# Optimization experiments

Hardware: AMD Instinct MI355X
Metric: run time of the kernel (lower is better)

The kernel has to match this reference:

```python
import jax, jax.numpy as jnp
import numpy as np

B, T, C, H, NT = 1, 1024, 768, 12, 8
D = C // H  # 64
POWER_ITERS = 4
DP_TEMP = 0.8
ESR_GAMMA = 0.02
ESR_ALPHA = 0.1


def rmsnorm(x, w, eps=1e-6):
    rms = jax.lax.rsqrt(jnp.mean(x * x, axis=-1, keepdims=True) + eps)
    return x * rms * w


def setup_inputs():
    key = jax.random.key(0)
    k0, k1, k2 = jax.random.split(key, 3)
    return {
        "x": jax.random.normal(k0, (B, T, C), jnp.float32),
        "W_qkvg": jax.random.normal(k1, (4 * C, C), jnp.float32) * 0.02,
        "W_out": jax.random.normal(k2, (C, C), jnp.float32) * 0.02,
        "lam": jnp.float32(1.5),
        "log_tau": -0.5 * jnp.ones((H, NT), jnp.float32),
        "logit_w": jnp.zeros((H, NT), jnp.float32),
        "beta": 1.5 * jnp.ones((H,), jnp.float32),
        "out_scale": jnp.ones((H,), jnp.float32),
        "dp_scale": jnp.ones((H,), jnp.float32),
        "logk_scale": jnp.ones((H,), jnp.float32),
        "dt_logit": jnp.float32(np.log(1.0 / 1e-8)),  # dt=1.0 -> logit = log(dt/(1-dt+1e-8))
        "g_norm_w": jnp.ones((D,), jnp.float32),
    }


def reference(x, W_qkvg, W_out, lam, log_tau, logit_w, beta, out_scale,
              dp_scale, logk_scale, dt_logit, g_norm_w):
    # qkvg projection and head split
    qkvg = x @ W_qkvg.T                                    # [B,T,4C]
    q, k, v, g = jnp.split(qkvg, 4, axis=-1)
    to_heads = lambda t: t.reshape(B, T, H, D).transpose(0, 2, 1, 3)  # [B,H,T,D]
    q, k, v, g = map(to_heads, (q, k, v, g))
    g = rmsnorm(g, g_norm_w)

    # pairwise squared distance ||g_i - g_j||^2
    g2 = jnp.sum(g * g, axis=-1)                           # [B,H,T]
    s = jnp.maximum(g2[..., :, None] + g2[..., None, :]
                    - 2.0 * jnp.einsum('bhid,bhjd->bhij', g, g), 0.0)  # [B,H,T,T]

    # fractional log-kernel: logsumexp_t[-(beta/2) log1p(s/(4 tau_t)) + log w_t]
    tau = jnp.maximum(jnp.exp(log_tau), 1e-6)              # [H,NT]
    w = jax.nn.softmax(logit_w, axis=-1)                   # [H,NT]
    beta_c = jnp.clip(beta, 0.5, 2.5)                      # [H]
    log_k_per = -(beta_c[None, :, None, None, None] / 2.0) * jnp.log1p(
        s[:, :, None] / (4.0 * tau[None, :, :, None, None]))          # [B,H,NT,T,T]
    logK = jax.nn.logsumexp(log_k_per + jnp.log(w + 1e-12)[None, :, :, None, None], axis=2)
    logK = logK * logk_scale[None, :, None, None]

    # dot-product scores
    dp = jnp.einsum('bhid,bhjd->bhij', q, k) * (dp_scale[None, :, None, None]
                                                / (np.sqrt(D) * DP_TEMP))

    # causal Markov normalize: blend, mask, stable row-softmax
    mask = jnp.tril(jnp.ones((T, T), bool))[None, None]    # [1,1,T,T]
    blended = lam * dp + (1.0 - lam) * logK
    blended = jnp.where(mask, blended, -jnp.inf)
    mx = jnp.max(blended, axis=-1, keepdims=True)
    mx = jnp.where(jnp.isfinite(mx), mx, 0.0)
    Kmat = jnp.exp(jnp.maximum(blended - mx, -60.0)) * mask
    P = Kmat / jnp.maximum(Kmat.sum(-1, keepdims=True), 1e-12)

    # power iteration for left stationary pi with full-support teleport
    pi0 = jnp.full((B, H, 1, T), 1.0 / T, P.dtype)
    def step(pi, _):
        p = (1.0 - ESR_GAMMA) * (pi @ P) + ESR_GAMMA / T
        p = p / jnp.maximum(p.sum(-1, keepdims=True), 1e-12)
        return p, None
    pi, _ = jax.lax.scan(step, pi0, None, length=POWER_ITERS)
    pi = jax.lax.stop_gradient(pi[..., 0, :])              # [B,H,T] (detached)

    # causal approximation to additive reversibilization
    P_adj = (pi[..., None, :] / jnp.maximum(pi[..., :, None], 1e-12)) \
            * jnp.swapaxes(P, -1, -2)                      # P*_ij = (pi_j/pi_i) P_ji
    P_rev = 0.5 * (P + P_adj) * mask
    P_rev = P_rev / jnp.maximum(P_rev.sum(-1, keepdims=True), 1e-12)

    dt = jax.nn.sigmoid(dt_logit)
    alpha = ESR_ALPHA * dt                                  # scale_alpha_by_dt=True
    P_fin = (1.0 - alpha) * P + alpha * P_rev

    y = (P_fin @ v) * out_scale[None, :, None, None]       # [B,H,T,D]
    y = y.transpose(0, 2, 1, 3).reshape(B, T, C)
    return y @ W_out.T
```

## Files before the change

### kernel.cpp

```cpp
#include <hip/hip_runtime.h>
#include <math.h>

#define TSEQ 1024
#define CD   768
#define HN   12
#define DD   64

#define OFF_QH     0
#define OFF_KH     393216
#define OFF_GH     786432
#define OFF_VHT    1179648
#define OFF_VH     1572864
#define OFF_G2     1966080
#define OFF_YB     1978368
#define OFF_CONSTS 2371584
#define OFF_OPART  2372096
#define OFF_LS     3158528
#define OFF_PD     3170816
#define OFF_XB     3183104
#define OFF_WQB    3576320
#define OFF_WOB    4755968
#define NZERO4     199680

#define N_XB  786432
#define N_WQB 2359296
#define N_WOB 589824

typedef __bf16 bf16x8 __attribute__((ext_vector_type(8)));
typedef float  f32x4  __attribute__((ext_vector_type(4)));
typedef unsigned short u16x8 __attribute__((ext_vector_type(8)));
typedef unsigned short u16x4 __attribute__((ext_vector_type(4)));

__device__ inline unsigned short f2bf(float f) {
  unsigned int u = __float_as_uint(f);
  return (unsigned short)((u + 0x7fffu + ((u >> 16) & 1u)) >> 16);
}
__device__ inline float bf2f(unsigned short u) {
  return __uint_as_float((unsigned)u << 16);
}


__global__ __launch_bounds__(64) void prep_kernel(
    const float* __restrict__ lam_p, const float* __restrict__ log_tau,
    const float* __restrict__ logit_w, const float* __restrict__ beta,
    const float* __restrict__ out_scale, const float* __restrict__ dp_scale,
    const float* __restrict__ logk_scale, const float* __restrict__ dt_logit,
    float* __restrict__ consts) {
  int h = threadIdx.x;
  if (h == 0) {
    float dt = 1.0f / (1.0f + __expf(-dt_logit[0]));
    consts[288] = 0.1f * dt;
  }
  if (h < HN) {
    float lam = lam_p[0];
    float* c = consts + h * 24;
    c[0] = lam * dp_scale[h] * (1.0f / 6.4f);
    c[1] = (1.0f - lam) * logk_scale[h];
    float b = fminf(fmaxf(beta[h], 0.5f), 2.5f);
    c[2] = 0.5f * b;
    c[3] = out_scale[h];
    float m = -1e30f;
    float lw[8];
    bool uni = true;
    for (int t = 0; t < 8; t++) {
      lw[t] = logit_w[h * 8 + t];
      m = fmaxf(m, lw[t]);
      if (log_tau[h * 8 + t] != log_tau[h * 8] || lw[t] != lw[0]) uni = false;
    }
    float s = 0.f;
    float e[8];
    for (int t = 0; t < 8; t++) { e[t] = __expf(lw[t] - m); s += e[t]; }
    for (int t = 0; t < 8; t++) {
      float w = e[t] / s;
      c[12 + t] = log2f(w + 1e-12f);
      float tau = fmaxf(__expf(log_tau[h * 8 + t]), 1e-6f);
      c[4 + t] = 1.0f / (4.0f * tau);
    }
    c[20] = uni ? 1.0f : 8.0f;
  }
}

__global__ __launch_bounds__(256) void zero_kernel(float4* __restrict__ p, int n4) {
  int i = blockIdx.x * 256 + threadIdx.x;
  for (; i < n4; i += gridDim.x * 256) p[i] = make_float4(0.f, 0.f, 0.f, 0.f);
}

__global__ __launch_bounds__(256) void convert_kernel(
    const float* __restrict__ x, const float* __restrict__ wq,
    const float* __restrict__ wo, unsigned short* __restrict__ xb,
    unsigned short* __restrict__ wqb, unsigned short* __restrict__ wob) {
  int i8 = (blockIdx.x * 256 + threadIdx.x) * 8;
  const float* src;
  unsigned short* dst;
  int off;
  if (i8 < N_XB) { src = x; dst = xb; off = i8; }
  else if (i8 < N_XB + N_WQB) { src = wq; dst = wqb; off = i8 - N_XB; }
  else if (i8 < N_XB + N_WQB + N_WOB) { src = wo; dst = wob; off = i8 - N_XB - N_WQB; }
  else return;
  float4 a = *(const float4*)&src[off];
  float4 b = *(const float4*)&src[off + 4];
  u16x8 u;
  u[0] = f2bf(a.x); u[1] = f2bf(a.y); u[2] = f2bf(a.z); u[3] = f2bf(a.w);
  u[4] = f2bf(b.x); u[5] = f2bf(b.y); u[6] = f2bf(b.z); u[7] = f2bf(b.w);
  *(u16x8*)&dst[off] = u;
}

__global__ __launch_bounds__(256, 2) void gemm_qkvg_fused(
    const unsigned short* __restrict__ A, const unsigned short* __restrict__ B,
    const float* __restrict__ consts, const float* __restrict__ g_norm_w,
    unsigned short* __restrict__ qh, unsigned short* __restrict__ kh,
    unsigned short* __restrict__ gh, unsigned short* __restrict__ vh,
    unsigned short* __restrict__ vhT, float* __restrict__ g2) {
  const int K = 768;
  __shared__ __align__(16) unsigned short As[128 * 72];
  __shared__ __align__(16) unsigned short Bs[64 * 72];
  int t = threadIdx.x;
  int lane = t & 63, w = t >> 6;
  int quad = lane >> 4, tx = lane & 15;
  int n0 = blockIdx.x * 64, m0 = blockIdx.y * 128;

  f32x4 acc[2][4] = {};
  int r_ = t >> 3, c8 = (t & 7) * 8;

  for (int k0 = 0; k0 < K; k0 += 64) {
    __syncthreads();
#pragma unroll
    for (int rep = 0; rep < 4; rep++) {
      int r = rep * 32 + r_;
      *(u16x8*)&As[r * 72 + c8] = *(const u16x8*)&A[(size_t)(m0 + r) * K + k0 + c8];
    }
#pragma unroll
    for (int rep = 0; rep < 2; rep++) {
      int r = rep * 32 + r_;
      *(u16x8*)&Bs[r * 72 + c8] = *(const u16x8*)&B[(size_t)(n0 + r) * K + k0 + c8];
    }
    __syncthreads();

#pragma unroll
    for (int ks = 0; ks < 2; ks++) {
      bf16x8 af[2];
#pragma unroll
      for (int mi = 0; mi < 2; mi++)
        af[mi] = *(const bf16x8*)&As[(32 * w + mi * 16 + tx) * 72 + ks * 32 + quad * 8];
#pragma unroll
      for (int ni = 0; ni < 4; ni++) {
        bf16x8 bv = *(const bf16x8*)&Bs[(ni * 16 + tx) * 72 + ks * 32 + quad * 8];
#pragma unroll
        for (int mi = 0; mi < 2; mi++)
          acc[mi][ni] = __builtin_amdgcn_mfma_f32_16x16x32_bf16(af[mi], bv, acc[mi][ni], 0, 0, 0);
      }
    }
  }

  int typ = n0 / CD;
  int h = (n0 - typ * CD) >> 6;
  unsigned short* Ls = As;
  __syncthreads();

  if (typ == 3) {
    float gw4[4];
#pragma unroll
    for (int ni = 0; ni < 4; ni++) gw4[ni] = g_norm_w[ni * 16 + tx];
#pragma unroll
    for (int mi = 0; mi < 2; mi++) {
#pragma unroll
      for (int reg = 0; reg < 4; reg++) {
        float s1 = acc[mi][0][reg] * acc[mi][0][reg] + acc[mi][1][reg] * acc[mi][1][reg]
                 + acc[mi][2][reg] * acc[mi][2][reg] + acc[mi][3][reg] * acc[mi][3][reg];
#pragma unroll
        for (int m = 1; m < 16; m <<= 1) s1 += __shfl_xor(s1, m, 64);
        float rms = rsqrtf(s1 * (1.f / 64.f) + 1e-6f);
        int rl = 32 * w + mi * 16 + quad * 4 + reg;
        float s2 = 0.f;
#pragma unroll
        for (int ni = 0; ni < 4; ni++) {
          float v = acc[mi][ni][reg] * rms * gw4[ni];
          unsigned short us = f2bf(v);
          Ls[rl * 72 + ni * 16 + tx] = us;
          float vb = bf2f(us);
          s2 += vb * vb;
        }
#pragma unroll
        for (int m = 1; m < 16; m <<= 1) s2 += __shfl_xor(s2, m, 64);
        if (tx == 0) g2[h * 1024 + m0 + rl] = s2;
      }
    }
    __syncthreads();
#pragma unroll
    for (int rep = 0; rep < 4; rep++) {
      int idx = rep * 256 + t;
      int r = idx >> 3, cc = (idx & 7) * 8;
      *(u16x8*)&gh[(size_t)(h * 1024 + m0 + r) * 64 + cc] = *(const u16x8*)&Ls[r * 72 + cc];
    }
  } else {
    float sc = (typ == 0) ? consts[h * 24] * 1.44269504089f : 1.0f;
#pragma unroll
    for (int mi = 0; mi < 2; mi++)
#pragma unroll
      for (int ni = 0; ni < 4; ni++)
#pragma unroll
        for (int reg = 0; reg < 4; reg++) {
          int rl = 32 * w + mi * 16 + quad * 4 + reg;
          Ls[rl * 72 + ni * 16 + tx] = f2bf(acc[mi][ni][reg] * sc);
        }
    __syncthreads();
    unsigned short* dst = (typ == 0) ? qh : ((typ == 1) ? kh : vh);
#pragma unroll
    for (int rep = 0; rep < 4; rep++) {
      int idx = rep * 256 + t;
      int r = idx >> 3, cc = (idx & 7) * 8;
      *(u16x8*)&dst[(size_t)(h * 1024 + m0 + r) * 64 + cc] = *(const u16x8*)&Ls[r * 72 + cc];
    }
    if (typ == 2) {
#pragma unroll
      for (int rep = 0; rep < 4; rep++) {
        int idx = rep * 256 + t;
        int d = idx >> 4, rc = (idx & 15) * 8;
        u16x8 u;
#pragma unroll
        for (int j = 0; j < 8; j++) u[j] = Ls[(rc + j) * 72 + d];
        *(u16x8*)&vhT[(size_t)(h * 64 + d) * 1024 + m0 + rc] = u;
      }
    }
  }
}

__global__ __launch_bounds__(256, 2) void gemm_bf16_abT(
    const unsigned short* __restrict__ A, const unsigned short* __restrict__ B,
    float* __restrict__ Cm, int M, int N, int K) {
  __shared__ __align__(16) unsigned short As[128 * 72];
  __shared__ __align__(16) unsigned short Bs[64 * 72];
  int t = threadIdx.x;
  int lane = t & 63, w = t >> 6;
  int quad = lane >> 4, tx = lane & 15;
  int n0 = blockIdx.x * 64, m0 = blockIdx.y * 128;

  f32x4 acc[2][4] = {};
  int r_ = t >> 3, c8 = (t & 7) * 8;

  for (int k0 = 0; k0 < K; k0 += 64) {
    __syncthreads();
#pragma unroll
    for (int rep = 0; rep < 4; rep++) {
      int r = rep * 32 + r_;
      *(u16x8*)&As[r * 72 + c8] = *(const u16x8*)&A[(size_t)(m0 + r) * K + k0 + c8];
    }
#pragma unroll
    for (int rep = 0; rep < 2; rep++) {
      int r = rep * 32 + r_;
      *(u16x8*)&Bs[r * 72 + c8] = *(const u16x8*)&B[(size_t)(n0 + r) * K + k0 + c8];
    }
    __syncthreads();

#pragma unroll
    for (int ks = 0; ks < 2; ks++) {
      bf16x8 af[2];
#pragma unroll
      for (int mi = 0; mi < 2; mi++)
        af[mi] = *(const bf16x8*)&As[(32 * w + mi * 16 + tx) * 72 + ks * 32 + quad * 8];
#pragma unroll
      for (int ni = 0; ni < 4; ni++) {
        bf16x8 bv = *(const bf16x8*)&Bs[(ni * 16 + tx) * 72 + ks * 32 + quad * 8];
#pragma unroll
        for (int mi = 0; mi < 2; mi++)
          acc[mi][ni] = __builtin_amdgcn_mfma_f32_16x16x32_bf16(af[mi], bv, acc[mi][ni], 0, 0, 0);
      }
    }
  }

#pragma unroll
  for (int mi = 0; mi < 2; mi++)
#pragma unroll
    for (int ni = 0; ni < 4; ni++)
#pragma unroll
      for (int reg = 0; reg < 4; reg++) {
        int row = m0 + 32 * w + mi * 16 + quad * 4 + reg;
        Cm[(size_t)row * N + n0 + ni * 16 + tx] = acc[mi][ni][reg];
      }
}

__global__ __launch_bounds__(256, 4) void flash_kernel(
    const unsigned short* __restrict__ qh, const unsigned short* __restrict__ kh,
    const unsigned short* __restrict__ gh, const unsigned short* __restrict__ vhT,
    const float* __restrict__ g2, const float* __restrict__ consts,
    float* __restrict__ Opart, float* __restrict__ lsp, float* __restrict__ pdp) {
  int h = blockIdx.y;
  int uu = 143 - (int)blockIdx.x;
  int it = 0, rem = uu;
  for (it = 0; it < 32; ++it) {
    int njt_ = (it >> 1) + 1;
    int nc = (njt_ + 1) >> 1;
    if (rem < nc) break;
    rem -= nc;
  }
  int njt = (it >> 1) + 1;
  int jt0 = rem * 2;
  int jt1 = (jt0 + 2 < njt) ? (jt0 + 2) : njt;
  bool owns_diag = (jt1 == njt);
  int i0 = it * 32;
  int t = threadIdx.x;
  int lane = t & 63, w = t >> 6;
  int quad = lane >> 4, tx = lane & 15;
  int mi = w >> 1, nb = (w & 1) * 2;

  __shared__ __align__(16) unsigned short Qa[32 * 72];
  __shared__ __align__(16) unsigned short Ga[32 * 72];
  __shared__ __align__(16) unsigned short Ks[64 * 72];
  __shared__ __align__(16) unsigned short GV[64 * 72];
  __shared__ __align__(16) unsigned short psh[32 * 72];
  __shared__ float g2i[32], g2j[64], pdiag[32];

  const float* ch = consts + h * 24;
  float lkc = ch[1], bh2 = ch[2];
  int ntt = (int)ch[20];
  float i4t0 = ch[4];
  float inv4tau[8], logw[8];
#pragma unroll
  for (int tt = 0; tt < 8; tt++) { inv4tau[tt] = ch[4 + tt]; logw[tt] = ch[12 + tt]; }

  {
    int r = t >> 3, c8 = (t & 7) * 8;
    *(u16x8*)&Qa[r * 72 + c8] = *(const u16x8*)&qh[(size_t)(h * 1024 + i0 + r) * 64 + c8];
    *(u16x8*)&Ga[r * 72 + c8] = *(const u16x8*)&gh[(size_t)(h * 1024 + i0 + r) * 64 + c8];
  }
  if (t < 32) { g2i[t] = g2[h * 1024 + i0 + t]; pdiag[t] = 0.f; }
  __syncthreads();

  bf16x8 aq[2], ag[2];
#pragma unroll
  for (int ks = 0; ks < 2; ks++) {
    aq[ks] = *(const bf16x8*)&Qa[(mi * 16 + tx) * 72 + ks * 32 + quad * 8];
    ag[ks] = *(const bf16x8*)&Ga[(mi * 16 + tx) * 72 + ks * 32 + quad * 8];
  }

  f32x4 Oc[2] = {};
  float rowacc[4] = {0.f, 0.f, 0.f, 0.f};
  int r4 = t >> 2, cb = (t & 3) * 16;

  for (int jt = jt0; jt < jt1; jt++) {
    int j0 = jt * 64;
    __syncthreads();
    {
      const unsigned short* kp = &kh[(size_t)(h * 1024 + j0 + r4) * 64 + cb];
      const unsigned short* gp = &gh[(size_t)(h * 1024 + j0 + r4) * 64 + cb];
      *(u16x8*)&Ks[r4 * 72 + cb] = *(const u16x8*)kp;
      *(u16x8*)&Ks[r4 * 72 + cb + 8] = *(const u16x8*)(kp + 8);
      *(u16x8*)&GV[r4 * 72 + cb] = *(const u16x8*)gp;
      *(u16x8*)&GV[r4 * 72 + cb + 8] = *(const u16x8*)(gp + 8);
    }
    if (t < 64) g2j[t] = g2[h * 1024 + j0 + t];
    __syncthreads();

    u16x8 v0, v1;
    {
      const unsigned short* vp = &vhT[(size_t)(h * 64 + r4) * 1024 + j0 + cb];
      v0 = *(const u16x8*)vp;
      v1 = *(const u16x8*)(vp + 8);
    }

    f32x4 sqk[2] = {}, sgg[2] = {};
#pragma unroll
    for (int ni2 = 0; ni2 < 2; ni2++) {
#pragma unroll
      for (int ks = 0; ks < 2; ks++) {
        bf16x8 bk = *(const bf16x8*)&Ks[((nb + ni2) * 16 + tx) * 72 + ks * 32 + quad * 8];
        sqk[ni2] = __builtin_amdgcn_mfma_f32_16x16x32_bf16(aq[ks], bk, sqk[ni2], 0, 0, 0);
        bf16x8 bg = *(const bf16x8*)&GV[((nb + ni2) * 16 + tx) * 72 + ks * 32 + quad * 8];
        sgg[ni2] = __builtin_amdgcn_mfma_f32_16x16x32_bf16(ag[ks], bg, sgg[ni2], 0, 0, 0);
      }
    }

    float rs[4] = {0.f, 0.f, 0.f, 0.f};
#pragma unroll
    for (int ni2 = 0; ni2 < 2; ni2++) {
      int colg = j0 + (nb + ni2) * 16 + tx;
      float g2jv = g2j[(nb + ni2) * 16 + tx];
#pragma unroll
      for (int reg = 0; reg < 4; reg++) {
        int rowl = mi * 16 + quad * 4 + reg;
        int gi = i0 + rowl;
        float s = fmaxf(g2i[rowl] + g2jv - 2.0f * sgg[ni2][reg], 0.0f);
        float lse2;
        if (ntt == 1) {
          lse2 = -bh2 * __builtin_amdgcn_logf(fmaf(s, i4t0, 1.0f));
        } else {
          float se = 0.f;
#pragma unroll
          for (int tt = 0; tt < 8; tt++) {
            float lv = __builtin_amdgcn_logf(fmaf(s, inv4tau[tt], 1.0f));
            se += __builtin_amdgcn_exp2f(fmaf(-bh2, lv, logw[tt]));
          }
          lse2 = __builtin_amdgcn_logf(se + 1e-30f);
        }
        float b = fmaf(lkc, lse2, sqk[ni2][reg]);
        float p = (colg <= gi) ? __builtin_amdgcn_exp2f(b) : 0.0f;
        rs[reg] += p;
        psh[rowl * 72 + (nb + ni2) * 16 + tx] = f2bf(p);
        if (colg == gi) pdiag[rowl] = p;
      }
    }
#pragma unroll
    for (int reg = 0; reg < 4; reg++) {
#pragma unroll
      for (int m = 1; m < 16; m <<= 1) rs[reg] += __shfl_xor(rs[reg], m, 64);
      rowacc[reg] += rs[reg];
    }
    __syncthreads();
    *(u16x8*)&GV[r4 * 72 + cb] = v0;
    *(u16x8*)&GV[r4 * 72 + cb + 8] = v1;
    __syncthreads();

    bf16x8 ap[2];
#pragma unroll
    for (int ks = 0; ks < 2; ks++)
      ap[ks] = *(const bf16x8*)&psh[(mi * 16 + tx) * 72 + ks * 32 + quad * 8];
#pragma unroll
    for (int nd2 = 0; nd2 < 2; nd2++) {
#pragma unroll
      for (int ks = 0; ks < 2; ks++) {
        bf16x8 bv = *(const bf16x8*)&GV[((nb + nd2) * 16 + tx) * 72 + ks * 32 + quad * 8];
        Oc[nd2] = __builtin_amdgcn_mfma_f32_16x16x32_bf16(ap[ks], bv, Oc[nd2], 0, 0, 0);
      }
    }
  }
  __syncthreads();

#pragma unroll
  for (int nd2 = 0; nd2 < 2; nd2++) {
#pragma unroll
    for (int reg = 0; reg < 4; reg++) {
      int row = i0 + mi * 16 + quad * 4 + reg;
      atomicAdd(&Opart[(size_t)(h * 1024 + row) * 64 + (nb + nd2) * 16 + tx], Oc[nd2][reg]);
    }
  }
  if (tx == 0) {
#pragma unroll
    for (int reg = 0; reg < 4; reg++)
      atomicAdd(&lsp[h * 1024 + i0 + mi * 16 + quad * 4 + reg], rowacc[reg]);
  }
  if (owns_diag && t < 32) pdp[h * 1024 + i0 + t] = pdiag[t];
}

__global__ __launch_bounds__(256) void finalize_kernel(
    const float* __restrict__ Opart, const float* __restrict__ lsp,
    const float* __restrict__ pdp, const unsigned short* __restrict__ vh,
    const float* __restrict__ consts, unsigned short* __restrict__ yb) {
  int h = blockIdx.y;
  int t = threadIdx.x;
  int rl = t >> 4, d4 = t & 15;
  int gi = blockIdx.x * 16 + rl;
  float alpha = consts[288];
  float osc = consts[h * 24 + 3];
  float l = fmaxf(lsp[h * TSEQ + gi], 1e-12f);
  float Pii = pdp[h * TSEQ + gi] / l;
  float inv1p = 1.0f / (1.0f + Pii);
  float c1 = (1.0f - alpha) + alpha * inv1p;
  float c2 = alpha * Pii * inv1p;
  float invl = 1.0f / l;
  float4 Ov = *(const float4*)&Opart[(size_t)(h * 1024 + gi) * 64 + 4 * d4];
  u16x4 vb = *(const u16x4*)&vh[(size_t)(h * 1024 + gi) * 64 + 4 * d4];
  u16x4 o;
  o[0] = f2bf(osc * (c1 * Ov.x * invl + c2 * bf2f(vb[0])));
  o[1] = f2bf(osc * (c1 * Ov.y * invl + c2 * bf2f(vb[1])));
  o[2] = f2bf(osc * (c1 * Ov.z * invl + c2 * bf2f(vb[2])));
  o[3] = f2bf(osc * (c1 * Ov.w * invl + c2 * bf2f(vb[3])));
  *(u16x4*)&yb[(size_t)gi * CD + h * 64 + 4 * d4] = o;
}

extern "C" void kernel_launch(void* const* d_in, const int* in_sizes, int n_in,
                              void* d_out, int out_size, void* d_ws, size_t ws_size,
                              hipStream_t stream) {
  (void)in_sizes; (void)n_in; (void)out_size; (void)ws_size;
  const float* x          = (const float*)d_in[0];
  const float* W_qkvg     = (const float*)d_in[1];
  const float* W_out      = (const float*)d_in[2];
  const float* lam        = (const float*)d_in[3];
  const float* log_tau    = (const float*)d_in[4];
  const float* logit_w    = (const float*)d_in[5];
  const float* beta       = (const float*)d_in[6];
  const float* out_scale  = (const float*)d_in[7];
  const float* dp_scale   = (const float*)d_in[8];
  const float* logk_scale = (const float*)d_in[9];
  const float* dt_logit   = (const float*)d_in[10];
  const float* g_norm_w   = (const float*)d_in[11];
  float* ws = (float*)d_ws;
  unsigned short* qh  = (unsigned short*)(ws + OFF_QH);
  unsigned short* kh  = (unsigned short*)(ws + OFF_KH);
  unsigned short* gh  = (unsigned short*)(ws + OFF_GH);
  unsigned short* vhT = (unsigned short*)(ws + OFF_VHT);
  unsigned short* vh  = (unsigned short*)(ws + OFF_VH);
  float* g2     = ws + OFF_G2;
  unsigned short* yb  = (unsigned short*)(ws + OFF_YB);
  float* consts = ws + OFF_CONSTS;
  float* Opart  = ws + OFF_OPART;
  float* lsp    = ws + OFF_LS;
  float* pdp    = ws + OFF_PD;
  unsigned short* xb  = (unsigned short*)(ws + OFF_XB);
  unsigned short* wqb = (unsigned short*)(ws + OFF_WQB);
  unsigned short* wob = (unsigned short*)(ws + OFF_WOB);
  float* out = (float*)d_out;

  prep_kernel<<<dim3(1), dim3(64), 0, stream>>>(lam, log_tau, logit_w, beta,
                                                out_scale, dp_scale, logk_scale,
                                                dt_logit, consts);
  zero_kernel<<<dim3(512), dim3(256), 0, stream>>>((float4*)Opart, NZERO4);
  convert_kernel<<<dim3((N_XB + N_WQB + N_WOB) / (256 * 8)), dim3(256), 0, stream>>>(
      x, W_qkvg, W_out, xb, wqb, wob);
  gemm_qkvg_fused<<<dim3(48, 8), dim3(256), 0, stream>>>(xb, wqb, consts, g_norm_w,
                                                         qh, kh, gh, vh, vhT, g2);
  flash_kernel<<<dim3(144, 12), dim3(256), 0, stream>>>(qh, kh, gh, vhT, g2, consts,
                                                        Opart, lsp, pdp);
  finalize_kernel<<<dim3(64, 12), dim3(256), 0, stream>>>(Opart, lsp, pdp, vh, consts, yb);
  gemm_bf16_abT<<<dim3(12, 8), dim3(256), 0, stream>>>(yb, wob, out, 1024, 768, 768);
}
```

Measured before the change: 163.2 us.

## Replace atomic partial-sum accumulation with per-chunk buffers reduced in finalize

The flash kernel now writes each split-K chunk's partial output and row sums into separate per-chunk slots instead of using float atomicAdd. The finalize kernel sums up to 8 chunks per row, which lets the zero-init kernel launch go away. The V tile is also staged into its own LDS buffer alongside K and G, so one sync/store round per tile is removed, and occupancy is lowered to 3 blocks per SM. The trade-off is more workspace memory and extra reads in finalize.

```diff
diff --git a/kernel.cpp b/kernel.cpp
--- a/kernel.cpp
+++ b/kernel.cpp
@@ -15,12 +15,11 @@
 #define OFF_YB     1978368
 #define OFF_CONSTS 2371584
 #define OFF_OPART  2372096
-#define OFF_LS     3158528
-#define OFF_PD     3170816
-#define OFF_XB     3183104
-#define OFF_WQB    3576320
-#define OFF_WOB    4755968
-#define NZERO4     199680
+#define OFF_LS     8663552
+#define OFF_PD     8761856
+#define OFF_XB     8774144
+#define OFF_WQB    9167360
+#define OFF_WOB    10347008
 
 #define N_XB  786432
 #define N_WQB 2359296
@@ -78,11 +77,6 @@
     }
     c[20] = uni ? 1.0f : 8.0f;
   }
-}
-
-__global__ __launch_bounds__(256) void zero_kernel(float4* __restrict__ p, int n4) {
-  int i = blockIdx.x * 256 + threadIdx.x;
-  for (; i < n4; i += gridDim.x * 256) p[i] = make_float4(0.f, 0.f, 0.f, 0.f);
 }
 
 __global__ __launch_bounds__(256) void convert_kernel(
@@ -279,7 +273,7 @@
       }
 }
 
-__global__ __launch_bounds__(256, 4) void flash_kernel(
+__global__ __launch_bounds__(256, 3) void flash_kernel(
     const unsigned short* __restrict__ qh, const unsigned short* __restrict__ kh,
     const unsigned short* __restrict__ gh, const unsigned short* __restrict__ vhT,
     const float* __restrict__ g2, const float* __restrict__ consts,
@@ -306,9 +300,10 @@
   __shared__ __align__(16) unsigned short Qa[32 * 72];
   __shared__ __align__(16) unsigned short Ga[32 * 72];
   __shared__ __align__(16) unsigned short Ks[64 * 72];
-  __shared__ __align__(16) unsigned short GV[64 * 72];
+  __shared__ __align__(16) unsigned short Gjs[64 * 72];
+  __shared__ __align__(16) unsigned short Vt[64 * 72];
   __shared__ __align__(16) unsigned short psh[32 * 72];
-  __shared__ float g2i[32], g2j[64], pdiag[32];
+  __shared__ float g2i[32], g2j[64], pdiag[32], lsum[32];
 
   const float* ch = consts + h * 24;
   float lkc = ch[1], bh2 = ch[2];
@@ -343,20 +338,16 @@
     {
       const unsigned short* kp = &kh[(size_t)(h * 1024 + j0 + r4) * 64 + cb];
       const unsigned short* gp = &gh[(size_t)(h * 1024 + j0 + r4) * 64 + cb];
+      const unsigned short* vp = &vhT[(size_t)(h * 64 + r4) * 1024 + j0 + cb];
       *(u16x8*)&Ks[r4 * 72 + cb] = *(const u16x8*)kp;
       *(u16x8*)&Ks[r4 * 72 + cb + 8] = *(const u16x8*)(kp + 8);
-      *(u16x8*)&GV[r4 * 72 + cb] = *(const u16x8*)gp;
-      *(u16x8*)&GV[r4 * 72 + cb + 8] = *(const u16x8*)(gp + 8);
+      *(u16x8*)&Gjs[r4 * 72 + cb] = *(const u16x8*)gp;
+      *(u16x8*)&Gjs[r4 * 72 + cb + 8] = *(const u16x8*)(gp + 8);
+      *(u16x8*)&Vt[r4 * 72 + cb] = *(const u16x8*)vp;
+      *(u16x8*)&Vt[r4 * 72 + cb + 8] = *(const u16x8*)(vp + 8);
     }
     if (t < 64) g2j[t] = g2[h * 1024 + j0 + t];
     __syncthreads();
-
-    u16x8 v0, v1;
-    {
-      const unsigned short* vp = &vhT[(size_t)(h * 64 + r4) * 1024 + j0 + cb];
-      v0 = *(const u16x8*)vp;
-      v1 = *(const u16x8*)(vp + 8);
-    }
 
     f32x4 sqk[2] = {}, sgg[2] = {};
 #pragma unroll
@@ -365,7 +356,7 @@
       for (int ks = 0; ks < 2; ks++) {
         bf16x8 bk = *(const bf16x8*)&Ks[((nb + ni2) * 16 + tx) * 72 + ks * 32 + quad * 8];
         sqk[ni2] = __builtin_amdgcn_mfma_f32_16x16x32_bf16(aq[ks], bk, sqk[ni2], 0, 0, 0);
-        bf16x8 bg = *(const bf16x8*)&GV[((nb + ni2) * 16 + tx) * 72 + ks * 32 + quad * 8];
+        bf16x8 bg = *(const bf16x8*)&Gjs[((nb + ni2) * 16 + tx) * 72 + ks * 32 + quad * 8];
         sgg[ni2] = __builtin_amdgcn_mfma_f32_16x16x32_bf16(ag[ks], bg, sgg[ni2], 0, 0, 0);
       }
     }
@@ -406,9 +397,6 @@
       rowacc[reg] += rs[reg];
     }
     __syncthreads();
-    *(u16x8*)&GV[r4 * 72 + cb] = v0;
-    *(u16x8*)&GV[r4 * 72 + cb + 8] = v1;
-    __syncthreads();
 
     bf16x8 ap[2];
 #pragma unroll
@@ -418,25 +406,32 @@
     for (int nd2 = 0; nd2 < 2; nd2++) {
 #pragma unroll
       for (int ks = 0; ks < 2; ks++) {
-        bf16x8 bv = *(const bf16x8*)&GV[((nb + nd2) * 16 + tx) * 72 + ks * 32 + quad * 8];
+        bf16x8 bv = *(const bf16x8*)&Vt[((nb + nd2) * 16 + tx) * 72 + ks * 32 + quad * 8];
         Oc[nd2] = __builtin_amdgcn_mfma_f32_16x16x32_bf16(ap[ks], bv, Oc[nd2], 0, 0, 0);
       }
     }
   }
+
+  if ((w & 1) == 0 && tx == 0) {
+#pragma unroll
+    for (int reg = 0; reg < 4; reg++) lsum[mi * 16 + quad * 4 + reg] = rowacc[reg];
+  }
   __syncthreads();
-
+  if ((w & 1) == 1 && tx == 0) {
+#pragma unroll
+    for (int reg = 0; reg < 4; reg++) {
+      int rowl = mi * 16 + quad * 4 + reg;
+      lsp[(size_t)(rem * HN + h) * 1024 + i0 + rowl] = lsum[rowl] + rowacc[reg];
+    }
+  }
+  float* Ob = Opart + (size_t)((rem * HN + h) * 1024 + i0) * 64;
 #pragma unroll
   for (int nd2 = 0; nd2 < 2; nd2++) {
 #pragma unroll
     for (int reg = 0; reg < 4; reg++) {
-      int row = i0 + mi * 16 + quad * 4 + reg;
-      atomicAdd(&Opart[(size_t)(h * 1024 + row) * 64 + (nb + nd2) * 16 + tx], Oc[nd2][reg]);
-    }
-  }
-  if (tx == 0) {
-#pragma unroll
-    for (int reg = 0; reg < 4; reg++)
-      atomicAdd(&lsp[h * 1024 + i0 + mi * 16 + quad * 4 + reg], rowacc[reg]);
+      int rowl = mi * 16 + quad * 4 + reg;
+      Ob[rowl * 64 + (nb + nd2) * 16 + tx] = Oc[nd2][reg];
+    }
   }
   if (owns_diag && t < 32) pdp[h * 1024 + i0 + t] = pdiag[t];
 }
@@ -449,15 +444,23 @@
   int t = threadIdx.x;
   int rl = t >> 4, d4 = t & 15;
   int gi = blockIdx.x * 16 + rl;
+  int it = gi >> 5;
+  int nc = (((it >> 1) + 1) + 1) >> 1;
   float alpha = consts[288];
   float osc = consts[h * 24 + 3];
-  float l = fmaxf(lsp[h * TSEQ + gi], 1e-12f);
+  float4 Ov = make_float4(0.f, 0.f, 0.f, 0.f);
+  float l = 0.f;
+  for (int c = 0; c < nc; c++) {
+    float4 p = *(const float4*)&Opart[(size_t)((c * HN + h) * 1024 + gi) * 64 + 4 * d4];
+    Ov.x += p.x; Ov.y += p.y; Ov.z += p.z; Ov.w += p.w;
+    l += lsp[(size_t)(c * HN + h) * 1024 + gi];
+  }
+  l = fmaxf(l, 1e-12f);
   float Pii = pdp[h * TSEQ + gi] / l;
   float inv1p = 1.0f / (1.0f + Pii);
   float c1 = (1.0f - alpha) + alpha * inv1p;
   float c2 = alpha * Pii * inv1p;
   float invl = 1.0f / l;
-  float4 Ov = *(const float4*)&Opart[(size_t)(h * 1024 + gi) * 64 + 4 * d4];
   u16x4 vb = *(const u16x4*)&vh[(size_t)(h * 1024 + gi) * 64 + 4 * d4];
   u16x4 o;
   o[0] = f2bf(osc * (c1 * Ov.x * invl + c2 * bf2f(vb[0])));
@@ -503,7 +506,6 @@
   prep_kernel<<<dim3(1), dim3(64), 0, stream>>>(lam, log_tau, logit_w, beta,
                                                 out_scale, dp_scale, logk_scale,
                                                 dt_logit, consts);
-  zero_kernel<<<dim3(512), dim3(256), 0, stream>>>((float4*)Opart, NZERO4);
   convert_kernel<<<dim3((N_XB + N_WQB + N_WOB) / (256 * 8)), dim3(256), 0, stream>>>(
       x, W_qkvg, W_out, xb, wqb, wob);
   gemm_qkvg_fused<<<dim3(48, 8), dim3(256), 0, stream>>>(xb, wqb, consts, g_norm_w,
```

Result: faster. 157.8 us (-3.3%).
